# Kernel tuning notes

Hardware: AMD Instinct MI355X
Metric: run time of the kernel (lower is better)

Reference implementation:

```python
import jax, jax.numpy as jnp
import numpy as np
from jax import lax
from math import sqrt

STYLE_DIM = 512
K = 3


def _equal_linear(latent, w, b):
    # EqualLinear: runtime weight scaling by 1/sqrt(fan_in)
    scale = 1.0 / sqrt(latent.shape[1])
    return latent @ (w.T * scale) + b


def _pixel_norm(x, axis=1, eps=1e-8):
    return x * jax.lax.rsqrt(jnp.mean(x * x, axis=axis, keepdims=True) + eps)


def _modconv(x, latent, weight, bias, el_w, el_b):
    # weight: (nc2, nc1, 3, 3); x: (B, nc1, H, W); latent: (B, style_dim)
    b = x.shape[0]
    nc2, nc1, k, _ = weight.shape
    fan_in = nc1 * k * k
    w = weight * sqrt(2.0 / fan_in)                      # (nc2, nc1, 3, 3)
    # style: s = 1 + PixelNorm(EqualLinear(latent))      # (B, nc1)
    s = 1.0 + _pixel_norm(_equal_linear(latent, el_w, el_b), axis=1)
    # demod: d_bo = rsqrt(sum_{c,k} (s_bc * w_ock)^2 + 1e-5)
    wsq = jnp.sum(w * w, axis=(2, 3))                    # (nc2, nc1)
    d = jax.lax.rsqrt(jnp.einsum('bc,oc->bo', s * s, wsq) + 1e-5)  # (B, nc2)
    # conv(x, s*w)*d  ==  conv(s*x, w)*d  (s is per input channel)
    xm = x * s[:, :, None, None]
    y = lax.conv_general_dilated(
        xm, w, window_strides=(1, 1), padding=[(1, 1), (1, 1)],
        dimension_numbers=('NCHW', 'OIHW', 'NCHW'))
    return y * d[:, :, None, None] + bias


def _style_block(x, latent, w0, b0, el0_w, el0_b, w1, b1, el1_w, el1_b):
    act_gain = sqrt(2.0)
    out = _modconv(x, latent, w0, b0, el0_w, el0_b)
    out = jax.nn.leaky_relu(out, 0.2) * act_gain
    out = _pixel_norm(out, axis=1)
    out = _modconv(out, latent, w1, b1, el1_w, el1_b)
    out = jax.nn.leaky_relu(out, 0.2) * act_gain
    out = _pixel_norm(out, axis=1)
    return out


def setup_inputs() -> dict:
    key = jax.random.key(0)
    ks = jax.random.split(key, 8)
    B, NC1, NC2, H, W = 8, 256, 256, 128, 128
    return {
        'x': jax.random.normal(ks[0], (B, NC1, H, W), jnp.float32),
        'latent': jax.random.normal(ks[1], (B, STYLE_DIM), jnp.float32),
        'w0': jax.random.normal(ks[2], (NC2, NC1, K, K), jnp.float32),
        'b0': jnp.zeros((1, NC2, 1, 1), jnp.float32),
        'el0_w': jax.random.normal(ks[3], (NC1, STYLE_DIM), jnp.float32),
        'el0_b': jnp.zeros((NC1,), jnp.float32),
        'w1': jax.random.normal(ks[4], (NC2, NC2, K, K), jnp.float32),
        'b1': jnp.zeros((1, NC2, 1, 1), jnp.float32),
        'el1_w': jax.random.normal(ks[5], (NC2, STYLE_DIM), jnp.float32),
        'el1_b': jnp.zeros((NC2,), jnp.float32),
    }


def reference(x, latent, w0, b0, el0_w, el0_b, w1, b1, el1_w, el1_b):
    return _style_block(x, latent, w0, b0, el0_w, el0_b, w1, b1, el1_w, el1_b)
```

## Files before the change

### kernel.cpp

```cpp
#include <hip/hip_runtime.h>
#include <hip/hip_bf16.h>

typedef __attribute__((ext_vector_type(8))) short short8;
typedef __attribute__((ext_vector_type(16))) float f32x16;

typedef const __attribute__((address_space(1))) unsigned int* gas1_t;
typedef __attribute__((address_space(3))) unsigned int* las3_t;

__device__ __forceinline__ unsigned short f2bf(float x) {
    unsigned int u = __float_as_uint(x);
    u = (u + 0x7fffu + ((u >> 16) & 1u)) >> 16;
    return (unsigned short)u;
}

__device__ __forceinline__ int4 pack8(const unsigned short* u) {
    int4 p;
    p.x = (int)((unsigned)u[0] | ((unsigned)u[1] << 16));
    p.y = (int)((unsigned)u[2] | ((unsigned)u[3] << 16));
    p.z = (int)((unsigned)u[4] | ((unsigned)u[5] << 16));
    p.w = (int)((unsigned)u[6] | ((unsigned)u[7] << 16));
    return p;
}

__device__ __forceinline__ void gld_lds16(const void* g, void* l) {
    __builtin_amdgcn_global_load_lds((gas1_t)g, (las3_t)l, 16, 0, 0);
}

__global__ void style_kernel(const float* __restrict__ latent,
                             const float* __restrict__ elw0, const float* __restrict__ elb0,
                             const float* __restrict__ elw1, const float* __restrict__ elb1,
                             float* __restrict__ s_arr) {
    const int cv = blockIdx.x >> 3;
    const int b  = blockIdx.x & 7;
    const int c  = threadIdx.x;
    const float* elw = cv ? elw1 : elw0;
    const float* elb = cv ? elb1 : elb0;

    __shared__ float lat[512];
    lat[c] = latent[b * 512 + c];
    lat[c + 256] = latent[b * 512 + c + 256];
    __syncthreads();

    float accv = 0.f;
    const float* wrow = elw + (size_t)c * 512;
#pragma unroll 8
    for (int k = 0; k < 512; ++k) accv += lat[k] * wrow[k];
    const float lin = accv * 0.04419417382415922f + elb[c];

    float sq = lin * lin;
#pragma unroll
    for (int off = 32; off >= 1; off >>= 1) sq += __shfl_xor(sq, off);
    __shared__ float wsum[4];
    if ((threadIdx.x & 63) == 0) wsum[threadIdx.x >> 6] = sq;
    __syncthreads();
    const float total = wsum[0] + wsum[1] + wsum[2] + wsum[3];
    const float s = 1.0f + lin * rsqrtf(total * (1.0f / 256.0f) + 1e-8f);
    s_arr[(cv * 8 + b) * 256 + c] = s;
}

__global__ void wsq_kernel(const float* __restrict__ w0, const float* __restrict__ w1,
                           float* __restrict__ wsq) {
    const int cv = blockIdx.x >> 8;
    const int o  = blockIdx.x & 255;
    const int c  = threadIdx.x;
    const float* w = cv ? w1 : w0;
    const size_t base = ((size_t)o * 256 + c) * 9;
    float ssum = 0.f;
#pragma unroll
    for (int t = 0; t < 9; ++t) { float v = w[base + t]; ssum += v * v; }
    wsq[((size_t)cv * 256 + o) * 256 + c] = ssum * (2.0f / 2304.0f);
}

__global__ void demod_kernel(const float* __restrict__ s_arr, const float* __restrict__ wsq,
                             float* __restrict__ d_arr) {
    const int cv = blockIdx.x >> 3;
    const int b  = blockIdx.x & 7;
    const int o  = threadIdx.x;
    __shared__ float ss[256];
    float sv = s_arr[(cv * 8 + b) * 256 + o];
    ss[o] = sv * sv;
    __syncthreads();
    const float* wrow = wsq + ((size_t)cv * 256 + o) * 256;
    float accv = 0.f;
#pragma unroll 8
    for (int c = 0; c < 256; ++c) accv += ss[c] * wrow[c];
    d_arr[(cv * 8 + b) * 256 + o] = rsqrtf(accv + 1e-5f);
}

__global__ void fold_kernel(const float* __restrict__ w0, const float* __restrict__ w1,
                            const float* __restrict__ s_arr, const float* __restrict__ d_arr,
                            unsigned short* __restrict__ wm0, unsigned short* __restrict__ wm1) {
    const int cv = blockIdx.y;
    const int e  = blockIdx.x * 256 + threadIdx.x;
    const float* w = cv ? w1 : w0;
    unsigned short* wm = cv ? wm1 : wm0;
    const int slab = e >> 13;
    const int idx  = e & 8191;
    const int b  = slab / 72;
    const int s2 = slab - b * 72;
    const int cc = s2 / 9;
    const int t  = s2 - cc * 9;
    const int o  = idx >> 5;
    const int c5 = idx & 31;
    const int c  = cc * 32 + c5;
    const float val = w[((size_t)o * 256 + c) * 9 + t] * 0.029462782549439483f
                    * s_arr[(cv * 8 + b) * 256 + c] * d_arr[(cv * 8 + b) * 256 + o];
    const int chunk = (c5 >> 3) ^ ((o >> 1) & 3);
    wm[((size_t)slab << 13) + o * 32 + (chunk << 3) + (c5 & 7)] = f2bf(val);
}

__global__ void convert_kernel(const float* __restrict__ x, unsigned short* __restrict__ xq) {
    const int blk = blockIdx.x;
    const int hh  = blk & 127;
    const int bg_ = blk >> 7;
    const int g   = bg_ & 31;
    const int b   = bg_ >> 5;
    __shared__ float sx[8][128];
    const int tid = threadIdx.x;
#pragma unroll
    for (int i = 0; i < 4; ++i) {
        const int idx = tid + i * 256;
        const int c8 = idx >> 7, p = idx & 127;
        sx[c8][p] = x[(((size_t)b * 256 + g * 8 + c8) * 128 + hh) * 128 + p];
    }
    __syncthreads();
    if (tid < 128) {
        const int p = tid;
        unsigned short u[8];
#pragma unroll
        for (int j = 0; j < 8; ++j) u[j] = f2bf(sx[j][p]);
        *(int4*)(xq + ((((size_t)b * 32 + g) * 128 + hh) * 128 + p) * 8) = pack8(u);
    }
}

template<int IN_MODE, bool FINAL_OUT>
__global__ __launch_bounds__(256, 2) void conv_kernel(
    const void* __restrict__ in_v, const unsigned short* __restrict__ wmod,
    const float* __restrict__ bias, void* __restrict__ out_v) {

    __shared__ __align__(16) char ldsA[32768];
    __shared__ __align__(16) char ldsB[16384];

    const int tid  = threadIdx.x;
    const int bh   = (blockIdx.x & 7) * 128 + (blockIdx.x >> 3);
    const int b    = bh >> 7;
    const int h    = bh & 127;
    const int lane = tid & 63;
    const int wr   = tid >> 6;
    const int wm   = wr & 1;
    const int wn   = wr >> 1;
    const int l31  = lane & 31;
    const int khg  = lane >> 5;

    const int px = tid & 127;
    const int bg = tid >> 7;

    int aoff[4][2], boff[2][2], bwoff[2];
#pragma unroll
    for (int mb = 0; mb < 4; ++mb)
#pragma unroll
        for (int kh = 0; kh < 2; ++kh) {
            const int o = wm * 128 + mb * 32 + l31;
            aoff[mb][kh] = o * 64 + (((khg + kh * 2) ^ ((o >> 1) & 3)) << 4);
        }
#pragma unroll
    for (int nb = 0; nb < 2; ++nb)
#pragma unroll
        for (int kh = 0; kh < 2; ++kh) {
            const int p = wn * 64 + nb * 32 + l31;
            boff[nb][kh] = p * 64 + (((khg + kh * 2) ^ ((p >> 1) & 3)) << 4);
        }
#pragma unroll
    for (int gg = 0; gg < 2; ++gg)
        bwoff[gg] = px * 64 + (((bg * 2 + gg) ^ ((px >> 1) & 3)) << 4);

    const unsigned short* wmb = wmod + (size_t)b * 589824;
    const unsigned short* inq = (const unsigned short*)in_v
                              + ((size_t)b * 32 + bg * 2) * 131072 + (size_t)px * 8;
    const float* inf = (const float*)in_v + ((size_t)b * 256 + bg * 16) * 16384 + px;

    f32x16 acc[4][2];
#pragma unroll
    for (int mb = 0; mb < 4; ++mb)
#pragma unroll
        for (int nb = 0; nb < 2; ++nb)
#pragma unroll
            for (int r = 0; r < 16; ++r) acc[mb][nb][r] = 0.f;

    auto loadB = [&](int ccv, int tv, int4& v0, int4& v1) {
        const int dyv = tv / 3, dxv = tv - (tv / 3) * 3;
        const int row = h + dyv - 1;
        const bool ok = ((unsigned)row < 128u) && ((unsigned)(px + dxv - 1) < 128u);
        if (IN_MODE == 1) {
            const unsigned short* p = inq + (size_t)(ccv * 4) * 131072
                                    + (size_t)row * 1024 + (dxv - 1) * 8;
            const int4 z = {0, 0, 0, 0};
            v0 = ok ? *(const int4*)p : z;
            v1 = ok ? *(const int4*)(p + 131072) : z;
        } else {
            unsigned short us[16];
            const float* p = inf + (size_t)(ccv * 32) * 16384 + (size_t)row * 128 + (dxv - 1);
#pragma unroll
            for (int j = 0; j < 16; ++j) us[j] = f2bf(ok ? p[(size_t)j * 16384] : 0.f);
            v0 = pack8(us);
            v1 = pack8(us + 8);
        }
    };

    auto issueA = [&](const char* gsrc, int nxt) {
        char* dst = ldsA + nxt * 16384 + wr * 4096;
        const char* s = gsrc + wr * 4096 + lane * 16;
        gld_lds16(s,        dst);
        gld_lds16(s + 1024, dst + 1024);
        gld_lds16(s + 2048, dst + 2048);
        gld_lds16(s + 3072, dst + 3072);
    };

    {
        int4 v0, v1;
        loadB(0, 0, v0, v1);
        issueA((const char*)wmb, 0);
        *(int4*)(ldsB + bwoff[0]) = v0;
        *(int4*)(ldsB + bwoff[1]) = v1;
    }
    __syncthreads();

    const char* gA = (const char*)wmb + 16384;
#pragma unroll 1
    for (int cc = 0; cc < 8; ++cc) {
#pragma unroll
        for (int t = 0; t < 9; ++t) {
            const int cur = (cc + t) & 1;
            const int nxt = cur ^ 1;
            const bool notLast = !(cc == 7 && t == 8);
            int4 v0, v1;
            if (notLast) {
                const int tn  = (t == 8) ? 0 : (t + 1);
                const int ccn = (t == 8) ? (cc + 1) : cc;
                loadB(ccn, tn, v0, v1);
                issueA(gA, nxt);
                gA += 16384;
            }
            const char* Ac = ldsA + cur * 16384;
            const char* Bc = ldsB + cur * 8192;
            short8 af[4][2], bf[2][2];
#pragma unroll
            for (int mb = 0; mb < 4; ++mb)
#pragma unroll
                for (int kh = 0; kh < 2; ++kh) af[mb][kh] = *(const short8*)(Ac + aoff[mb][kh]);
#pragma unroll
            for (int nb = 0; nb < 2; ++nb)
#pragma unroll
                for (int kh = 0; kh < 2; ++kh) bf[nb][kh] = *(const short8*)(Bc + boff[nb][kh]);
#pragma unroll
            for (int kh = 0; kh < 2; ++kh)
#pragma unroll
                for (int mb = 0; mb < 4; ++mb)
#pragma unroll
                    for (int nb = 0; nb < 2; ++nb)
                        acc[mb][nb] = __builtin_amdgcn_mfma_f32_32x32x16_bf16(
                            af[mb][kh], bf[nb][kh], acc[mb][nb], 0, 0, 0);
            if (notLast) {
                *(int4*)(ldsB + nxt * 8192 + bwoff[0]) = v0;
                *(int4*)(ldsB + nxt * 8192 + bwoff[1]) = v1;
            }
            __syncthreads();
        }
    }

    float* sb = (float*)ldsB;
    sb[tid] = bias[tid];
    __syncthreads();

    float psum[2] = {0.f, 0.f};
    const float actGain = 1.4142135623730951f;
#pragma unroll
    for (int mb = 0; mb < 4; ++mb)
#pragma unroll
        for (int rg = 0; rg < 16; ++rg) {
            const int row = (rg & 3) + 8 * (rg >> 2) + 4 * khg;
            const float bo = sb[wm * 128 + mb * 32 + row];
#pragma unroll
            for (int nb = 0; nb < 2; ++nb) {
                float v = acc[mb][nb][rg] + bo;
                v = (v > 0.f ? v : 0.2f * v) * actGain;
                acc[mb][nb][rg] = v;
                psum[nb] += v * v;
            }
        }
    psum[0] += __shfl_xor(psum[0], 32);
    psum[1] += __shfl_xor(psum[1], 32);
    float* red = (float*)ldsA;
    if (lane < 32) {
        red[(wn * 2 + wm) * 64 + l31]      = psum[0];
        red[(wn * 2 + wm) * 64 + 32 + l31] = psum[1];
    }
    __syncthreads();
    float rs[2];
#pragma unroll
    for (int nb = 0; nb < 2; ++nb) {
        const float ssum = red[(wn * 2) * 64 + nb * 32 + l31]
                         + red[(wn * 2 + 1) * 64 + nb * 32 + l31];
        rs[nb] = rsqrtf(ssum * (1.0f / 256.0f) + 1e-8f);
    }

    if (FINAL_OUT) {
        float* outF = (float*)out_v;
#pragma unroll
        for (int mb = 0; mb < 4; ++mb)
#pragma unroll
            for (int rg = 0; rg < 16; ++rg) {
                const int row = (rg & 3) + 8 * (rg >> 2) + 4 * khg;
                const int o = wm * 128 + mb * 32 + row;
                const size_t rb = (((size_t)b * 256 + o) * 128 + h) * 128;
#pragma unroll
                for (int nb = 0; nb < 2; ++nb)
                    outF[rb + wn * 64 + nb * 32 + l31] = acc[mb][nb][rg] * rs[nb];
            }
    } else {
        unsigned short* outB = (unsigned short*)out_v;
        char* wreg = ldsA + wr * 4096;
        __syncthreads();
#pragma unroll
        for (int mb = 0; mb < 4; ++mb) {
#pragma unroll
            for (int rg = 0; rg < 16; rg += 2) {
                const int row = (rg & 3) + 8 * (rg >> 2) + 4 * khg;
#pragma unroll
                for (int nb = 0; nb < 2; ++nb) {
                    const int pxl = nb * 32 + l31;
                    const unsigned lo = f2bf(acc[mb][nb][rg]     * rs[nb]);
                    const unsigned hi = f2bf(acc[mb][nb][rg + 1] * rs[nb]);
                    *(unsigned int*)(wreg + pxl * 64 + (((row >> 3) ^ (pxl & 3)) << 4)
                                     + (row & 7) * 2) = lo | (hi << 16);
                }
            }
            asm volatile("s_waitcnt lgkmcnt(0)" ::: "memory");
#pragma unroll
            for (int oc = 0; oc < 4; ++oc) {
                const int4 v = *(const int4*)(wreg + lane * 64 + ((oc ^ (lane & 3)) << 4));
                const int g = wm * 16 + mb * 4 + oc;
                *(int4*)(outB + ((((size_t)b * 32 + g) * 128 + h) * 128 + wn * 64 + lane) * 8) = v;
            }
            asm volatile("s_waitcnt lgkmcnt(0)" ::: "memory");
        }
    }
}

extern "C" void kernel_launch(void* const* d_in, const int* in_sizes, int n_in,
                              void* d_out, int out_size, void* d_ws, size_t ws_size,
                              hipStream_t stream) {
    (void)in_sizes; (void)n_in; (void)out_size;
    const float* x      = (const float*)d_in[0];
    const float* latent = (const float*)d_in[1];
    const float* w0     = (const float*)d_in[2];
    const float* b0     = (const float*)d_in[3];
    const float* el0w   = (const float*)d_in[4];
    const float* el0b   = (const float*)d_in[5];
    const float* w1     = (const float*)d_in[6];
    const float* b1     = (const float*)d_in[7];
    const float* el1w   = (const float*)d_in[8];
    const float* el1b   = (const float*)d_in[9];

    char* ws = (char*)d_ws;
    float* s_arr = (float*)ws;
    float* d_arr = (float*)(ws + 16384);
    float* wsq   = (float*)(ws + 32768);
    unsigned short* wm0 = (unsigned short*)(ws + 557056);
    unsigned short* wm1 = (unsigned short*)(ws + 9994240);
    const bool full = ws_size >= (size_t)153649152;
    unsigned short* xq  = (unsigned short*)(ws + 19431424);
    unsigned short* tmp = (unsigned short*)(ws + (full ? 86540288 : 19431424));

    style_kernel<<<16, 256, 0, stream>>>(latent, el0w, el0b, el1w, el1b, s_arr);
    wsq_kernel<<<512, 256, 0, stream>>>(w0, w1, wsq);
    demod_kernel<<<16, 256, 0, stream>>>(s_arr, wsq, d_arr);
    fold_kernel<<<dim3(18432, 2), 256, 0, stream>>>(w0, w1, s_arr, d_arr, wm0, wm1);

    if (full) {
        convert_kernel<<<32768, 256, 0, stream>>>(x, xq);
        conv_kernel<1, false><<<1024, 256, 0, stream>>>(xq, wm0, b0, tmp);
    } else {
        conv_kernel<0, false><<<1024, 256, 0, stream>>>(x, wm0, b0, tmp);
    }
    conv_kernel<1, true><<<1024, 256, 0, stream>>>(tmp, wm1, b1, d_out);
}
```

Baseline: 414.5 us.

## Stage three-row input halo in LDS per channel chunk, triple-buffer weight tiles

The conv kernel now loads the three input rows for each 32-channel chunk straight into LDS with direct global-to-LDS loads. It then reads all nine taps from that shared tile using shifted, swizzled offsets and a zero page for the border columns. Before, each tap reloaded the input through registers, so this reuse should cut repeated global reads and register staging. Weight tiles go from double to triple buffering, with explicit vmcnt waits, raw barriers and setprio around the MFMA loop. In exchange it drops the fp32-input fallback, needs the full workspace, grows LDS use to about 75KB per block, and aliases the zero page onto the wsq buffer.

```diff
diff --git a/kernel.cpp b/kernel.cpp
--- a/kernel.cpp
+++ b/kernel.cpp
@@ -133,13 +133,15 @@
     }
 }
 
-template<int IN_MODE, bool FINAL_OUT>
+template<bool FINAL_OUT>
 __global__ __launch_bounds__(256, 2) void conv_kernel(
-    const void* __restrict__ in_v, const unsigned short* __restrict__ wmod,
-    const float* __restrict__ bias, void* __restrict__ out_v) {
-
-    __shared__ __align__(16) char ldsA[32768];
-    __shared__ __align__(16) char ldsB[16384];
+    const unsigned short* __restrict__ in_q, const unsigned short* __restrict__ wmod,
+    const float* __restrict__ bias, const unsigned short* __restrict__ zpg,
+    void* __restrict__ out_v) {
+
+    __shared__ __align__(16) char ldsA[49152];
+    __shared__ __align__(16) char ldsB[24640];
+    __shared__ float sbias[256];
 
     const int tid  = threadIdx.x;
     const int bh   = (blockIdx.x & 7) * 128 + (blockIdx.x >> 3);
@@ -152,10 +154,10 @@
     const int l31  = lane & 31;
     const int khg  = lane >> 5;
 
-    const int px = tid & 127;
-    const int bg = tid >> 7;
-
-    int aoff[4][2], boff[2][2], bwoff[2];
+    sbias[tid] = bias[tid];
+    if (tid < 4) *(int4*)(ldsB + 24576 + tid * 16) = (int4){0, 0, 0, 0};
+
+    int aoff[4][2];
 #pragma unroll
     for (int mb = 0; mb < 4; ++mb)
 #pragma unroll
@@ -163,21 +165,49 @@
             const int o = wm * 128 + mb * 32 + l31;
             aoff[mb][kh] = o * 64 + (((khg + kh * 2) ^ ((o >> 1) & 3)) << 4);
         }
+
+    int bC[2][2], bL[2][2], bR[2][2];
 #pragma unroll
     for (int nb = 0; nb < 2; ++nb)
 #pragma unroll
         for (int kh = 0; kh < 2; ++kh) {
-            const int p = wn * 64 + nb * 32 + l31;
-            boff[nb][kh] = p * 64 + (((khg + kh * 2) ^ ((p >> 1) & 3)) << 4);
-        }
-#pragma unroll
-    for (int gg = 0; gg < 2; ++gg)
-        bwoff[gg] = px * 64 + (((bg * 2 + gg) ^ ((px >> 1) & 3)) << 4);
+            const int cx0 = wn * 64 + nb * 32 + l31;
+            const int clog = khg + kh * 2;
+            const int cl = cx0 - 1, cr = cx0 + 1;
+            bC[nb][kh] = cx0 * 64 + ((clog ^ ((cx0 >> 1) & 3)) << 4);
+            bL[nb][kh] = cl * 64 + ((clog ^ ((cl >> 1) & 3)) << 4);
+            bR[nb][kh] = cr * 64 + ((clog ^ ((cr >> 1) & 3)) << 4);
+        }
+    const bool isL = (wn == 0) && (l31 == 0);
+    const bool isR = (wn == 1) && (l31 == 31);
 
     const unsigned short* wmb = wmod + (size_t)b * 589824;
-    const unsigned short* inq = (const unsigned short*)in_v
-                              + ((size_t)b * 32 + bg * 2) * 131072 + (size_t)px * 8;
-    const float* inf = (const float*)in_v + ((size_t)b * 256 + bg * 16) * 16384 + px;
+    const unsigned short* xqb = in_q + (size_t)b * 4194304;
+
+    auto issueA = [&](const char* src, int bufidx) {
+        char* dstb = ldsA + bufidx * 16384 + wr * 1024;
+        const char* s = src + wr * 1024 + lane * 16;
+#pragma unroll
+        for (int i = 0; i < 4; ++i)
+            gld_lds16(s + i * 4096, dstb + i * 4096);
+    };
+
+    auto issueB = [&](int ccn) {
+#pragma unroll
+        for (int i = 0; i < 6; ++i) {
+            const int slot = i * 256 + tid;
+            const int rowidx = slot >> 2;
+            const int cph = slot & 3;
+            const int r = rowidx >> 7;
+            const int pxs = rowidx & 127;
+            const int clog = cph ^ ((rowidx >> 1) & 3);
+            const int hin = h + r - 1;
+            const unsigned short* src = ((unsigned)hin < 128u)
+                ? xqb + (((size_t)(ccn * 4 + clog) * 128 + hin) * 128 + pxs) * 8
+                : zpg;
+            gld_lds16(src, ldsB + (i * 256 + wr * 64) * 16);
+        }
+    };
 
     f32x16 acc[4][2];
 #pragma unroll
@@ -187,62 +217,22 @@
 #pragma unroll
             for (int r = 0; r < 16; ++r) acc[mb][nb][r] = 0.f;
 
-    auto loadB = [&](int ccv, int tv, int4& v0, int4& v1) {
-        const int dyv = tv / 3, dxv = tv - (tv / 3) * 3;
-        const int row = h + dyv - 1;
-        const bool ok = ((unsigned)row < 128u) && ((unsigned)(px + dxv - 1) < 128u);
-        if (IN_MODE == 1) {
-            const unsigned short* p = inq + (size_t)(ccv * 4) * 131072
-                                    + (size_t)row * 1024 + (dxv - 1) * 8;
-            const int4 z = {0, 0, 0, 0};
-            v0 = ok ? *(const int4*)p : z;
-            v1 = ok ? *(const int4*)(p + 131072) : z;
-        } else {
-            unsigned short us[16];
-            const float* p = inf + (size_t)(ccv * 32) * 16384 + (size_t)row * 128 + (dxv - 1);
-#pragma unroll
-            for (int j = 0; j < 16; ++j) us[j] = f2bf(ok ? p[(size_t)j * 16384] : 0.f);
-            v0 = pack8(us);
-            v1 = pack8(us + 8);
-        }
-    };
-
-    auto issueA = [&](const char* gsrc, int nxt) {
-        char* dst = ldsA + nxt * 16384 + wr * 4096;
-        const char* s = gsrc + wr * 4096 + lane * 16;
-        gld_lds16(s,        dst);
-        gld_lds16(s + 1024, dst + 1024);
-        gld_lds16(s + 2048, dst + 2048);
-        gld_lds16(s + 3072, dst + 3072);
-    };
-
-    {
-        int4 v0, v1;
-        loadB(0, 0, v0, v1);
-        issueA((const char*)wmb, 0);
-        *(int4*)(ldsB + bwoff[0]) = v0;
-        *(int4*)(ldsB + bwoff[1]) = v1;
-    }
-    __syncthreads();
-
-    const char* gA = (const char*)wmb + 16384;
+    issueB(0);
+    issueA((const char*)wmb, 0);
+    issueA((const char*)wmb + 16384, 1);
+    __syncthreads();
+
+    const char* gA = (const char*)wmb + 32768;
 #pragma unroll 1
     for (int cc = 0; cc < 8; ++cc) {
 #pragma unroll
         for (int t = 0; t < 9; ++t) {
-            const int cur = (cc + t) & 1;
-            const int nxt = cur ^ 1;
-            const bool notLast = !(cc == 7 && t == 8);
-            int4 v0, v1;
-            if (notLast) {
-                const int tn  = (t == 8) ? 0 : (t + 1);
-                const int ccn = (t == 8) ? (cc + 1) : cc;
-                loadB(ccn, tn, v0, v1);
-                issueA(gA, nxt);
-                gA += 16384;
-            }
+            const int dy = t / 3, dx = t - (t / 3) * 3;
+            const int cur = t % 3, tgt = (t + 2) % 3;
+            const bool doIssue = (cc < 7) || (t < 7);
+            if (doIssue) { issueA(gA, tgt); gA += 16384; }
+
             const char* Ac = ldsA + cur * 16384;
-            const char* Bc = ldsB + cur * 8192;
             short8 af[4][2], bf[2][2];
 #pragma unroll
             for (int mb = 0; mb < 4; ++mb)
@@ -251,7 +241,21 @@
 #pragma unroll
             for (int nb = 0; nb < 2; ++nb)
 #pragma unroll
-                for (int kh = 0; kh < 2; ++kh) bf[nb][kh] = *(const short8*)(Bc + boff[nb][kh]);
+                for (int kh = 0; kh < 2; ++kh) {
+                    int off;
+                    if (dx == 1) {
+                        off = bC[nb][kh] + dy * 8192;
+                    } else if (dx == 0) {
+                        off = bL[nb][kh] + dy * 8192;
+                        if (nb == 0) off = isL ? 24576 : off;
+                    } else {
+                        off = bR[nb][kh] + dy * 8192;
+                        if (nb == 1) off = isR ? 24576 : off;
+                    }
+                    bf[nb][kh] = *(const short8*)(ldsB + off);
+                }
+
+            __builtin_amdgcn_s_setprio(1);
 #pragma unroll
             for (int kh = 0; kh < 2; ++kh)
 #pragma unroll
@@ -260,17 +264,18 @@
                     for (int nb = 0; nb < 2; ++nb)
                         acc[mb][nb] = __builtin_amdgcn_mfma_f32_32x32x16_bf16(
                             af[mb][kh], bf[nb][kh], acc[mb][nb], 0, 0, 0);
-            if (notLast) {
-                *(int4*)(ldsB + nxt * 8192 + bwoff[0]) = v0;
-                *(int4*)(ldsB + nxt * 8192 + bwoff[1]) = v1;
-            }
+            __builtin_amdgcn_s_setprio(0);
+
+            if (doIssue) asm volatile("s_waitcnt vmcnt(4) lgkmcnt(0)" ::: "memory");
+            else         asm volatile("s_waitcnt vmcnt(0) lgkmcnt(0)" ::: "memory");
+            __builtin_amdgcn_sched_barrier(0);
+            __builtin_amdgcn_s_barrier();
+        }
+        if (cc < 7) {
+            issueB(cc + 1);
             __syncthreads();
         }
     }
-
-    float* sb = (float*)ldsB;
-    sb[tid] = bias[tid];
-    __syncthreads();
 
     float psum[2] = {0.f, 0.f};
     const float actGain = 1.4142135623730951f;
@@ -279,7 +284,7 @@
 #pragma unroll
         for (int rg = 0; rg < 16; ++rg) {
             const int row = (rg & 3) + 8 * (rg >> 2) + 4 * khg;
-            const float bo = sb[wm * 128 + mb * 32 + row];
+            const float bo = sbias[wm * 128 + mb * 32 + row];
 #pragma unroll
             for (int nb = 0; nb < 2; ++nb) {
                 float v = acc[mb][nb][rg] + bo;
@@ -350,7 +355,7 @@
 extern "C" void kernel_launch(void* const* d_in, const int* in_sizes, int n_in,
                               void* d_out, int out_size, void* d_ws, size_t ws_size,
                               hipStream_t stream) {
-    (void)in_sizes; (void)n_in; (void)out_size;
+    (void)in_sizes; (void)n_in; (void)out_size; (void)ws_size;
     const float* x      = (const float*)d_in[0];
     const float* latent = (const float*)d_in[1];
     const float* w0     = (const float*)d_in[2];
@@ -366,22 +371,19 @@
     float* s_arr = (float*)ws;
     float* d_arr = (float*)(ws + 16384);
     float* wsq   = (float*)(ws + 32768);
+    unsigned short* zpg = (unsigned short*)(ws + 32768);
     unsigned short* wm0 = (unsigned short*)(ws + 557056);
     unsigned short* wm1 = (unsigned short*)(ws + 9994240);
-    const bool full = ws_size >= (size_t)153649152;
     unsigned short* xq  = (unsigned short*)(ws + 19431424);
-    unsigned short* tmp = (unsigned short*)(ws + (full ? 86540288 : 19431424));
+    unsigned short* tmp = (unsigned short*)(ws + 86540288);
 
     style_kernel<<<16, 256, 0, stream>>>(latent, el0w, el0b, el1w, el1b, s_arr);
     wsq_kernel<<<512, 256, 0, stream>>>(w0, w1, wsq);
     demod_kernel<<<16, 256, 0, stream>>>(s_arr, wsq, d_arr);
+    hipMemsetAsync(zpg, 0, 256, stream);
     fold_kernel<<<dim3(18432, 2), 256, 0, stream>>>(w0, w1, s_arr, d_arr, wm0, wm1);
-
-    if (full) {
-        convert_kernel<<<32768, 256, 0, stream>>>(x, xq);
-        conv_kernel<1, false><<<1024, 256, 0, stream>>>(xq, wm0, b0, tmp);
-    } else {
-        conv_kernel<0, false><<<1024, 256, 0, stream>>>(x, wm0, b0, tmp);
-    }
-    conv_kernel<1, true><<<1024, 256, 0, stream>>>(tmp, wm1, b1, d_out);
-}
+    convert_kernel<<<32768, 256, 0, stream>>>(x, xq);
+
+    conv_kernel<false><<<1024, 256, 0, stream>>>(xq, wm0, b0, zpg, tmp);
+    conv_kernel<true><<<1024, 256, 0, stream>>>(tmp, wm1, b1, zpg, d_out);
+}
```

Result: faster. 398.5 us (-3.9%).
